# Kernel optimization log

Measured on AMD Instinct MI355X. Metric: run time of the kernel, lower is better.

The kernel has to match this reference:

```python
import jax, jax.numpy as jnp
import numpy as np

STRIDE = 16
SCALES = (0.5, 1.0, 2.0)
RATIOS = (0.5, 1.0, 2.0)
IOU_THR = 0.7
CONF_THR = 0.5
KEEP_PRE = 6000
KEEP_POST = 300


def _default_boxes(fh, fw):
    # anchors centered at origin: size = stride*scale, w/h set by aspect ratio
    s = STRIDE * jnp.asarray(SCALES, jnp.float32)                    # [S]
    r = jnp.asarray(RATIOS, jnp.float32)                             # [R]
    w = (s[None, :] * jnp.sqrt(1.0 / r)[:, None]).reshape(-1)        # [A]
    h = (s[None, :] * jnp.sqrt(r)[:, None]).reshape(-1)              # [A]
    anchors = jnp.stack([-w / 2, -h / 2, w / 2, h / 2], axis=-1)     # [A,4]
    sx = jnp.arange(fw, dtype=jnp.float32) * STRIDE
    sy = jnp.arange(fh, dtype=jnp.float32) * STRIDE
    gx, gy = jnp.meshgrid(sx, sy)                                    # [fh,fw]
    shifts = jnp.stack([gx, gy, gx, gy], axis=-1)                    # [fh,fw,4]
    return (shifts[:, :, None, :] + anchors[None, None, :, :]).reshape(-1, 4)


def _apply_regs(deltas, boxes):
    # deltas: [bs,N,4] (dx,dy,dw,dh); boxes: [N,4] xyxy default boxes
    w = boxes[:, 2] - boxes[:, 0]
    h = boxes[:, 3] - boxes[:, 1]
    cx = boxes[:, 0] + 0.5 * w
    cy = boxes[:, 1] + 0.5 * h
    pcx = deltas[..., 0] * w + cx
    pcy = deltas[..., 1] * h + cy
    pw = jnp.exp(deltas[..., 2]) * w
    ph = jnp.exp(deltas[..., 3]) * h
    return jnp.stack([pcx - 0.5 * pw, pcy - 0.5 * ph,
                      pcx + 0.5 * pw, pcy + 0.5 * ph], axis=-1)


def _clip(boxes, img_h, img_w):
    lim = jnp.asarray([img_w, img_h, img_w, img_h], jnp.float32)
    return jnp.clip(boxes, 0.0, lim)


def _pairwise_iou(b):
    area = jnp.maximum(b[:, 2] - b[:, 0], 0.0) * jnp.maximum(b[:, 3] - b[:, 1], 0.0)
    lt = jnp.maximum(b[:, None, :2], b[None, :, :2])
    rb = jnp.minimum(b[:, None, 2:], b[None, :, 2:])
    wh = jnp.maximum(rb - lt, 0.0)
    inter = wh[..., 0] * wh[..., 1]
    union = area[:, None] + area[None, :] - inter
    return inter / jnp.maximum(union, 1e-9)


def _nms_keep(boxes, thr):
    # boxes are pre-sorted by descending score -> greedy NMS == row sweep
    n = boxes.shape[0]
    iou = _pairwise_iou(jax.lax.stop_gradient(boxes))  # [n,n]
    idx = jnp.arange(n)
    def body(i, keep):
        sup = (iou[i] > thr) & (idx > i)
        return keep & jnp.where(keep[i], ~sup, True)
    return jax.lax.fori_loop(0, n, body, jnp.ones(n, dtype=bool))


def _detect_one(boxes, scores):
    order = jnp.argsort(-scores)
    props = boxes[order][:KEEP_PRE]          # [P,4]
    sc = scores[order][:KEEP_PRE]            # [P]
    keep = _nms_keep(props, IOU_THR)
    pos = jnp.cumsum(keep) - 1               # compacted position of kept boxes
    valid = keep & (pos < KEEP_POST)
    dst = jnp.where(valid, pos, KEEP_POST)   # out-of-range -> dropped by scatter
    out_b = jnp.zeros((KEEP_POST, 4), props.dtype).at[dst].set(props, mode='drop')
    out_s = jnp.zeros((KEEP_POST,), sc.dtype).at[dst].set(sc, mode='drop')
    # confidence filter: zero out rows below threshold (fixed-shape analog of list)
    return out_b * (out_s > CONF_THR).astype(props.dtype)[:, None]


def reference(preds, regs, img_h, img_w):
    bs, fh, fw, na = preds.shape
    db = _default_boxes(fh, fw)                          # [fh*fw*A, 4]
    scores = jax.nn.sigmoid(preds).reshape(bs, -1)       # [bs, N]
    boxes = _apply_regs(regs.reshape(bs, -1, 4), db)     # [bs, N, 4]
    boxes = _clip(boxes, img_h, img_w)
    outs = [_detect_one(boxes[i], scores[i]) for i in range(bs)]
    return jnp.stack(outs)                               # [bs, KEEP_POST, 4]


def setup_inputs() -> dict:
    key = jax.random.key(0)
    k1, k2 = jax.random.split(key)
    preds = jax.random.normal(k1, (4, 37, 62, 9), jnp.float32)
    regs = jax.random.normal(k2, (4, 37, 62, 9, 4), jnp.float32)
    return {"preds": preds, "regs": regs, "img_h": 600, "img_w": 1000}
```

## Files before the change

### kernel.cpp

```cpp
#include <hip/hip_runtime.h>
#include <stdint.h>

typedef unsigned long long u64;
typedef unsigned int u32;

#define FH 37
#define FW 62
#define NA 9
#define NPRED 20646
#define BS 4
#define KEEP_PRE 6000
#define KEEP_POST 300
#define NBINS 4096
#define SELCAP 3072
#define SLOTN 6144
#define FB_BASE 4608
#define NFB 640
#define NCHUNK 21
#define FSLOTS 32
#define FSUB 64

#define L_HIST   0u
#define L_SUF    16384u
#define L_RG1    32768u
#define L_RG2    81920u
#define L_FBCUR  106496u
#define L_PERM   109056u
#define L_KBOX   121344u
#define L_KAREA  126208u
#define L_WSUM   127424u
#define L_WPOS   127488u
#define L_SCAL   127552u
#define L_AW     127616u
#define L_MROW   127872u
#define LDS_TOTAL 128384u

__device__ __forceinline__ u32 mapbits(float p) {
  u32 u = __float_as_uint(p);
  return (u & 0x80000000u) ? ~u : (u | 0x80000000u);
}
__device__ __forceinline__ u64 readlane64(u64 v, int srcLane) {
  u32 lo = __builtin_amdgcn_readlane((u32)v, srcLane);
  u32 hi = __builtin_amdgcn_readlane((u32)(v >> 32), srcLane);
  return ((u64)hi << 32) | lo;
}
__device__ __forceinline__ bool iou_sup(float kx1, float ky1, float kx2, float ky2,
                                        float ka, float cx1, float cy1,
                                        float cx2, float cy2, float ca) {
  float wx = fmaxf(fminf(kx2, cx2) - fmaxf(kx1, cx1), 0.f);
  float wy = fmaxf(fminf(ky2, cy2) - fmaxf(ky1, cy1), 0.f);
  float inter = wx * wy;
  float un = ka + ca - inter;
  return inter > 0.7f * fmaxf(un, 1e-9f);
}
__device__ __forceinline__ float4 decode_box(u32 n, float4 d, float W, float H) {
  int a = (int)(n % NA);
  int cell = (int)(n / NA);
  int x = cell % FW;
  int y = cell / FW;
  int si = a % 3, ri = a / 3;
  float s = (si==0) ? 8.f : ((si==1) ? 16.f : 32.f);
  float r = (ri==0) ? 0.5f : ((ri==1) ? 1.0f : 2.0f);
  float aw = s * sqrtf(1.0f / r);
  float ah = s * sqrtf(r);
  float gx = (float)x * 16.f, gy = (float)y * 16.f;
  float x1d = gx - 0.5f*aw, x2d = gx + 0.5f*aw;
  float y1d = gy - 0.5f*ah, y2d = gy + 0.5f*ah;
  float w = x2d - x1d, h = y2d - y1d;
  float cx = x1d + 0.5f*w, cy = y1d + 0.5f*h;
  float pcx = d.x*w + cx, pcy = d.y*h + cy;
  float pw = expf(d.z)*w, ph = expf(d.w)*h;
  float bx1 = fminf(fmaxf(pcx - 0.5f*pw, 0.f), W);
  float by1 = fminf(fmaxf(pcy - 0.5f*ph, 0.f), H);
  float bx2 = fminf(fmaxf(pcx + 0.5f*pw, 0.f), W);
  float by2 = fminf(fmaxf(pcy + 0.5f*ph, 0.f), H);
  return make_float4(bx1, by1, bx2, by2);
}

__global__ void __launch_bounds__(1024) detect_kernel(
    const float* __restrict__ preds, const float4* __restrict__ regs4,
    const int* __restrict__ ih, const int* __restrict__ iw,
    float4* __restrict__ out)
{
  __shared__ __align__(16) char smem[LDS_TOTAL];
  u32*    histL  = (u32*)(smem + L_HIST);
  u32*    sufL   = (u32*)(smem + L_SUF);
  u32*    repl   = (u32*)(smem + L_RG1);
  u64*    slots  = (u64*)(smem + L_RG1);
  float4* cboxL  = (float4*)(smem + L_RG1);
  u32*    fineH  = (u32*)(smem + L_RG2);
  u32*    fineS  = (u32*)(smem + L_RG2 + 8192);
  u32*    fineC  = (u32*)(smem + L_RG2 + 16384);
  float*  careaL = (float*)(smem + L_RG2);
  u32*    fbCur  = (u32*)(smem + L_FBCUR);
  u32*    perm   = (u32*)(smem + L_PERM);
  float4* kbox   = (float4*)(smem + L_KBOX);
  float*  karea  = (float*)(smem + L_KAREA);
  u32*    wsum   = (u32*)(smem + L_WSUM);
  u32*    wpos   = (u32*)(smem + L_WPOS);
  u32*    scal   = (u32*)(smem + L_SCAL);
  u64*    aw     = (u64*)(smem + L_AW);
  u64*    mrow   = (u64*)(smem + L_MROW);

  const int b = blockIdx.x;
  const int t = threadIdx.x;
  const int lane = t & 63;
  const int wv = t >> 6;
  const float* pb = preds + b*NPRED;
  const float4* rb = regs4 + b*NPRED;
  const float W = (float)(*iw), H = (float)(*ih);
  float4* ob = out + b*KEEP_POST;
  const float4 zero = make_float4(0.f, 0.f, 0.f, 0.f);

  #pragma unroll
  for (int q = 0; q < 4; ++q) histL[q*1024 + t] = 0;
  #pragma unroll
  for (int q = 0; q < 12; ++q) repl[q*1024 + t] = 0;
  if (t == 0) scal[2] = 0;
  __syncthreads();

  {
    u32* repA = ((wv & 3) == 0) ? histL : (repl + ((wv & 3) - 1) * 4096);
    u32 mypos = 0;
    #pragma unroll 4
    for (int c = 0; c < NCHUNK; ++c) {
      int n = c*1024 + t;
      bool valid = (n < NPRED);
      float p = valid ? pb[n] : -1.0f;
      u64 bm = __ballot(valid && (p > 0.0f));
      mypos += (u32)__popcll(bm);
      if (valid) atomicAdd(&repA[mapbits(p) >> 20], 1u);
    }
    if (lane == 0) wpos[wv] = mypos;
  }
  __syncthreads();

  {
    u32* r2 = repl + 4096; u32* r3 = repl + 8192;
    u32 h0 = histL[4*t+0] + repl[4*t+0] + r2[4*t+0] + r3[4*t+0];
    u32 h1 = histL[4*t+1] + repl[4*t+1] + r2[4*t+1] + r3[4*t+1];
    u32 h2 = histL[4*t+2] + repl[4*t+2] + r2[4*t+2] + r3[4*t+2];
    u32 h3 = histL[4*t+3] + repl[4*t+3] + r2[4*t+3] + r3[4*t+3];
    histL[4*t+0]=h0; histL[4*t+1]=h1; histL[4*t+2]=h2; histL[4*t+3]=h3;
    u32 s = h0 + h1 + h2 + h3;
    u32 sf = s;
    #pragma unroll
    for (int off = 1; off < 64; off <<= 1) {
      u32 o = __shfl_down(sf, off, 64);
      if (lane + off < 64) sf += o;
    }
    if (lane == 0) wsum[wv] = sf;
    __syncthreads();
    u32 hi = 0;
    #pragma unroll
    for (int w2 = 0; w2 < 16; ++w2) hi += (w2 > wv) ? wsum[w2] : 0u;
    u32 St = hi + (sf - s);
    u32 s3 = St, s2 = s3 + h3, s1 = s2 + h2, s0 = s1 + h1;
    sufL[4*t+0]=s0; sufL[4*t+1]=s1; sufL[4*t+2]=s2; sufL[4*t+3]=s3;
    if (t == 0) {
      u32 np = 0;
      #pragma unroll
      for (int w2 = 0; w2 < 16; ++w2) np += wpos[w2];
      scal[3] = np;
    }
  }
  __syncthreads();

  #pragma unroll 1
  for (int tr = 0; tr < 2; ++tr) {
    const u32 winStart = (u32)tr * SELCAP;
    const u32 winEnd = winStart + SELCAP;
    const int rowLimit = (KEEP_PRE - (int)winStart < (int)SELCAP)
                           ? (KEEP_PRE - (int)winStart) : (int)SELCAP;

    if (t == 0) { scal[0] = 0xFFFFFFFFu; scal[1] = 0u; }
    __syncthreads();
    #pragma unroll
    for (int q = 0; q < 4; ++q) {
      int v = 4*t + q;
      u32 hv = histL[v], sv = sufL[v];
      if (hv && sv < winEnd && sv + hv > winStart) {
        atomicMin(&scal[0], (u32)v);
        atomicMax(&scal[1], (u32)v);
      }
    }
    __syncthreads();
    const u32 binLo = scal[0], binHi = scal[1];
    u32 cBase = binLo;
    if (binHi - binLo >= FSLOTS) cBase = binHi - (FSLOTS - 1);
    const u32 S_top = sufL[binHi];
    const u32 S_cb = (cBase > 0) ? sufL[cBase-1] : 0;
    const u32 rebWinEnd = winEnd - S_top;

    #pragma unroll
    for (int q = 0; q < 2; ++q) fineH[q*1024 + t] = 0;
    #pragma unroll
    for (int q = 0; q < 6; ++q) slots[q*1024 + t] = 0ull;
    if (t < NFB) {
      u32 v = binLo + (u32)t;
      fbCur[t] = (v < cBase) ? (FB_BASE + (sufL[v] - S_cb)) : (u32)SLOTN;
    }
    __syncthreads();

    #pragma unroll 4
    for (int c = 0; c < NCHUNK; ++c) {
      int n = c*1024 + t;
      if (n < NPRED) {
        u32 m = mapbits(pb[n]);
        u32 cb = m >> 20;
        if (cb >= cBase && cb <= binHi)
          atomicAdd(&fineH[((cb - cBase) << 6) | ((m >> 14) & 0x3F)], 1u);
      }
    }
    __syncthreads();

    {
      u32 f0 = fineH[2*t], f1 = fineH[2*t+1];
      u32 s = f0 + f1;
      u32 sf = s;
      #pragma unroll
      for (int off = 1; off < 64; off <<= 1) {
        u32 o = __shfl_down(sf, off, 64);
        if (lane + off < 64) sf += o;
      }
      if (lane == 0) wsum[wv] = sf;
      __syncthreads();
      u32 hi = 0;
      #pragma unroll
      for (int w2 = 0; w2 < 16; ++w2) hi += (w2 > wv) ? wsum[w2] : 0u;
      u32 St = hi + (sf - s);
      u32 sA = St + f1, sB = St;
      fineS[2*t] = sA; fineS[2*t+1] = sB;
      fineC[2*t] = sA; fineC[2*t+1] = sB;
    }
    __syncthreads();

    #pragma unroll 4
    for (int c = 0; c < NCHUNK; ++c) {
      int n = c*1024 + t;
      if (n < NPRED) {
        u32 m = mapbits(pb[n]);
        u32 cb = m >> 20;
        u64 key = ((u64)m << 32) | (u32)(~(u32)n);
        if (cb >= cBase && cb <= binHi) {
          u32 F = ((cb - cBase) << 6) | ((m >> 14) & 0x3F);
          if (fineS[F] < rebWinEnd) {
            u32 pos = atomicAdd(&fineC[F], 1u);
            if (pos < FB_BASE) slots[pos] = key;
          }
        } else if (cb >= binLo && cb < cBase) {
          u32 fo = cb - binLo;
          if (fo < NFB) {
            u32 pos = atomicAdd(&fbCur[fo], 1u);
            if (pos < SLOTN) slots[pos] = key;
          }
        }
      }
    }
    __syncthreads();

    #pragma unroll
    for (int q = 0; q < 6; ++q) {
      int i = q*1024 + t;
      u64 k = slots[i];
      if (k != 0) {
        u32 m = (u32)(k >> 32);
        u32 cb = m >> 20;
        u32 base, end, rbase;
        if (cb >= cBase) {
          u32 F = ((cb - cBase) << 6) | ((m >> 14) & 0x3F);
          base = fineS[F];
          end = base + fineH[F]; if (end > FB_BASE) end = FB_BASE;
          rbase = S_top + fineS[F];
        } else {
          base = FB_BASE + (sufL[cb] - S_cb);
          end = base + histL[cb]; if (end > SLOTN) end = SLOTN;
          rbase = sufL[cb];
        }
        u32 c2 = 0;
        for (u32 j = base; j < end; j += 4) {
          u64 s0 = slots[j];
          u64 s1 = (j+1 < end) ? slots[j+1] : 0ull;
          u64 s2 = (j+2 < end) ? slots[j+2] : 0ull;
          u64 s3 = (j+3 < end) ? slots[j+3] : 0ull;
          c2 += (u32)(s0 > k) + (u32)(s1 > k) + (u32)(s2 > k) + (u32)(s3 > k);
        }
        int local = (int)(rbase + c2) - (int)winStart;
        if (local >= 0 && local < rowLimit) perm[local] = ~(u32)k;
      }
    }
    __syncthreads();

    for (int r = t; r < rowLimit; r += 1024) {
      u32 idx = perm[r];
      float4 bx = decode_box(idx, rb[idx], W, H);
      cboxL[r] = bx;
      careaL[r] = (bx.z - bx.x) * (bx.w - bx.y);
    }
    __syncthreads();

    {
      const int npos = (int)scal[3];
      const int nblk = (rowLimit + 63) >> 6;
      for (int blk = 0; blk < nblk; ++blk) {
        int cnt = (int)scal[2];
        if (cnt >= KEEP_POST) break;
        const int base = blk * 64;
        const int ci = base + lane;
        const bool valid = (ci < rowLimit);
        float4 cur = cboxL[valid ? ci : 0];
        float carea = careaL[valid ? ci : 0];

        int dead = 0;
        #pragma unroll 2
        for (int k = wv; k < cnt; k += 16) {
          float4 kb = kbox[k];
          dead |= (int)iou_sup(kb.x, kb.y, kb.z, kb.w, karea[k],
                               cur.x, cur.y, cur.z, cur.w, carea);
        }
        u64* awb = aw + ((blk & 1) << 4);
        awb[wv] = __ballot(dead);
        __syncthreads();

        u64 deadAll = 0;
        #pragma unroll
        for (int k = 0; k < 16; ++k) deadAll |= awb[k];
        int rem = rowLimit - base;
        u64 vm = (rem >= 64) ? ~0ull : ((1ull << rem) - 1ull);
        u64 A = vm & ~deadAll;
        if (A == 0) continue;

        #pragma unroll
        for (int q = 0; q < 4; ++q) {
          int j = wv*4 + q;
          if ((A >> j) & 1ull) {
            float4 bj = cboxL[base + j];
            float ja = careaL[base + j];
            bool s = iou_sup(bj.x, bj.y, bj.z, bj.w, ja,
                             cur.x, cur.y, cur.z, cur.w, carea);
            u64 bm = __ballot(s);
            if (lane == 0) mrow[j] = bm;
          } else if (lane == 0) {
            mrow[j] = 0ull;
          }
        }
        __syncthreads();

        if (wv == 0) {
          u64 mreg = mrow[lane];
          int c2 = cnt;
          while (A && c2 < KEEP_POST) {
            int j = (int)__builtin_ctzll(A);
            A &= A - 1;
            A &= ~readlane64(mreg, j);
            if (lane == 0) {
              float4 bj = cboxL[base + j];
              kbox[c2] = bj;
              karea[c2] = careaL[base + j];
              ob[c2] = ((int)(winStart + (u32)(base + j)) < npos) ? bj : zero;
            }
            ++c2;
          }
          if (lane == 0) scal[2] = (u32)c2;
        }
        __syncthreads();
      }
    }
    __syncthreads();
    if ((int)scal[2] >= KEEP_POST) break;
  }

  for (int k2 = (int)scal[2] + t; k2 < KEEP_POST; k2 += 1024) ob[k2] = zero;
}

extern "C" void kernel_launch(void* const* d_in, const int* in_sizes, int n_in,
                              void* d_out, int out_size, void* d_ws, size_t ws_size,
                              hipStream_t stream) {
  const float* preds  = (const float*)d_in[0];
  const float4* regs4 = (const float4*)d_in[1];
  const int* ih       = (const int*)d_in[2];
  const int* iw       = (const int*)d_in[3];
  (void)d_ws; (void)ws_size; (void)in_sizes; (void)n_in; (void)out_size;

  detect_kernel<<<dim3(BS), 1024, 0, stream>>>(
      preds, regs4, ih, iw, (float4*)d_out);
}
```

Baseline: 174.2 us.

## Compact window candidates, split sort keys, lazily decode boxes, merge NMS barriers

The histogram pass now uses a single LDS histogram with no wave replicas, and the positive count is reduced with shuffles. The fine-histogram pass compacts in-window candidates into an LDS list through ballot and atomic offsets, so the scatter pass no longer rereads all predictions from global memory. Sort keys are split into 32-bit score bits plus 16-bit indices to save LDS. Box decoding is done for the first 1024 rows up front and the rest only when NMS reaches them. The intra-block suppression matrix is computed alongside the dead-mask pass so one barrier per block is removed, at the cost of always computing all 64 rows.

```diff
diff --git a/kernel.cpp b/kernel.cpp
--- a/kernel.cpp
+++ b/kernel.cpp
@@ -3,6 +3,7 @@
 
 typedef unsigned long long u64;
 typedef unsigned int u32;
+typedef unsigned short u16;
 
 #define FH 37
 #define FW 62
@@ -20,20 +21,27 @@
 #define FSLOTS 32
 #define FSUB 64
 
-#define L_HIST   0u
-#define L_SUF    16384u
-#define L_RG1    32768u
-#define L_RG2    81920u
-#define L_FBCUR  106496u
-#define L_PERM   109056u
-#define L_KBOX   121344u
-#define L_KAREA  126208u
-#define L_WSUM   127424u
-#define L_WPOS   127488u
-#define L_SCAL   127552u
-#define L_AW     127616u
-#define L_MROW   127872u
-#define LDS_TOTAL 128384u
+#define L_HIST    0u
+#define L_SUF     16384u
+#define L_C       32768u
+#define L_CM      (L_C + 0u)
+#define L_CN      (L_C + 24576u)
+#define L_FINEH   (L_C + 36864u)
+#define L_FINES   (L_C + 45056u)
+#define L_FINEC   (L_C + 53248u)
+#define L_FBCUR   (L_C + 61440u)
+#define L_CBOX    (L_C + 0u)
+#define L_CAREA   (L_C + 49152u)
+#define L_SLOTM   96768u
+#define L_SLOTN   121344u
+#define L_PERM    133632u
+#define L_KBOX    145920u
+#define L_KAREA   150720u
+#define L_WSUM    151920u
+#define L_SCAL    151984u
+#define L_AW      152016u
+#define L_MROW    152272u
+#define LDS_TOTAL 152832u
 
 __device__ __forceinline__ u32 mapbits(float p) {
   u32 u = __float_as_uint(p);
@@ -85,19 +93,20 @@
   __shared__ __align__(16) char smem[LDS_TOTAL];
   u32*    histL  = (u32*)(smem + L_HIST);
   u32*    sufL   = (u32*)(smem + L_SUF);
-  u32*    repl   = (u32*)(smem + L_RG1);
-  u64*    slots  = (u64*)(smem + L_RG1);
-  float4* cboxL  = (float4*)(smem + L_RG1);
-  u32*    fineH  = (u32*)(smem + L_RG2);
-  u32*    fineS  = (u32*)(smem + L_RG2 + 8192);
-  u32*    fineC  = (u32*)(smem + L_RG2 + 16384);
-  float*  careaL = (float*)(smem + L_RG2);
+  u32*    compM  = (u32*)(smem + L_CM);
+  u16*    compN  = (u16*)(smem + L_CN);
+  u32*    fineH  = (u32*)(smem + L_FINEH);
+  u32*    fineS  = (u32*)(smem + L_FINES);
+  u32*    fineC  = (u32*)(smem + L_FINEC);
   u32*    fbCur  = (u32*)(smem + L_FBCUR);
+  float4* cboxL  = (float4*)(smem + L_CBOX);
+  float*  careaL = (float*)(smem + L_CAREA);
+  u32*    slotM  = (u32*)(smem + L_SLOTM);
+  u16*    slotN  = (u16*)(smem + L_SLOTN);
   u32*    perm   = (u32*)(smem + L_PERM);
   float4* kbox   = (float4*)(smem + L_KBOX);
   float*  karea  = (float*)(smem + L_KAREA);
   u32*    wsum   = (u32*)(smem + L_WSUM);
-  u32*    wpos   = (u32*)(smem + L_WPOS);
   u32*    scal   = (u32*)(smem + L_SCAL);
   u64*    aw     = (u64*)(smem + L_AW);
   u64*    mrow   = (u64*)(smem + L_MROW);
@@ -112,57 +121,42 @@
   float4* ob = out + b*KEEP_POST;
   const float4 zero = make_float4(0.f, 0.f, 0.f, 0.f);
 
-  #pragma unroll
-  for (int q = 0; q < 4; ++q) histL[q*1024 + t] = 0;
-  #pragma unroll
-  for (int q = 0; q < 12; ++q) repl[q*1024 + t] = 0;
-  if (t == 0) scal[2] = 0;
+  ((uint4*)histL)[t] = make_uint4(0,0,0,0);
+  if (t == 0) { scal[2] = 0; scal[3] = 0; }
   __syncthreads();
 
-  {
-    u32* repA = ((wv & 3) == 0) ? histL : (repl + ((wv & 3) - 1) * 4096);
-    u32 mypos = 0;
-    #pragma unroll 4
-    for (int c = 0; c < NCHUNK; ++c) {
-      int n = c*1024 + t;
-      bool valid = (n < NPRED);
-      float p = valid ? pb[n] : -1.0f;
-      u64 bm = __ballot(valid && (p > 0.0f));
-      mypos += (u32)__popcll(bm);
-      if (valid) atomicAdd(&repA[mapbits(p) >> 20], 1u);
-    }
-    if (lane == 0) wpos[wv] = mypos;
+  u32 mypos = 0;
+  #pragma unroll 4
+  for (int c = 0; c < NCHUNK; ++c) {
+    int n = c*1024 + t;
+    if (n < NPRED) {
+      float p = pb[n];
+      mypos += (p > 0.0f) ? 1u : 0u;
+      atomicAdd(&histL[mapbits(p) >> 20], 1u);
+    }
   }
   __syncthreads();
 
   {
-    u32* r2 = repl + 4096; u32* r3 = repl + 8192;
-    u32 h0 = histL[4*t+0] + repl[4*t+0] + r2[4*t+0] + r3[4*t+0];
-    u32 h1 = histL[4*t+1] + repl[4*t+1] + r2[4*t+1] + r3[4*t+1];
-    u32 h2 = histL[4*t+2] + repl[4*t+2] + r2[4*t+2] + r3[4*t+2];
-    u32 h3 = histL[4*t+3] + repl[4*t+3] + r2[4*t+3] + r3[4*t+3];
-    histL[4*t+0]=h0; histL[4*t+1]=h1; histL[4*t+2]=h2; histL[4*t+3]=h3;
-    u32 s = h0 + h1 + h2 + h3;
+    uint4 h = ((const uint4*)histL)[t];
+    u32 s = h.x + h.y + h.z + h.w;
     u32 sf = s;
+    u32 mp = mypos;
     #pragma unroll
     for (int off = 1; off < 64; off <<= 1) {
       u32 o = __shfl_down(sf, off, 64);
       if (lane + off < 64) sf += o;
-    }
-    if (lane == 0) wsum[wv] = sf;
+      mp += __shfl_down(mp, off, 64);
+    }
+    if (lane == 0) { wsum[wv] = sf; atomicAdd(&scal[3], mp); }
     __syncthreads();
     u32 hi = 0;
     #pragma unroll
     for (int w2 = 0; w2 < 16; ++w2) hi += (w2 > wv) ? wsum[w2] : 0u;
     u32 St = hi + (sf - s);
-    u32 s3 = St, s2 = s3 + h3, s1 = s2 + h2, s0 = s1 + h1;
-    sufL[4*t+0]=s0; sufL[4*t+1]=s1; sufL[4*t+2]=s2; sufL[4*t+3]=s3;
-    if (t == 0) {
-      u32 np = 0;
-      #pragma unroll
-      for (int w2 = 0; w2 < 16; ++w2) np += wpos[w2];
-      scal[3] = np;
-    }
+    uint4 sv;
+    sv.w = St; sv.z = St + h.w; sv.y = sv.z + h.z; sv.x = sv.y + h.y;
+    ((uint4*)sufL)[t] = sv;
   }
   __syncthreads();
 
@@ -173,7 +167,7 @@
     const int rowLimit = (KEEP_PRE - (int)winStart < (int)SELCAP)
                            ? (KEEP_PRE - (int)winStart) : (int)SELCAP;
 
-    if (t == 0) { scal[0] = 0xFFFFFFFFu; scal[1] = 0u; }
+    if (t == 0) { scal[0] = 0xFFFFFFFFu; scal[1] = 0u; scal[4] = 0u; }
     __syncthreads();
     #pragma unroll
     for (int q = 0; q < 4; ++q) {
@@ -191,25 +185,42 @@
     const u32 S_top = sufL[binHi];
     const u32 S_cb = (cBase > 0) ? sufL[cBase-1] : 0;
     const u32 rebWinEnd = winEnd - S_top;
-
-    #pragma unroll
-    for (int q = 0; q < 2; ++q) fineH[q*1024 + t] = 0;
-    #pragma unroll
-    for (int q = 0; q < 6; ++q) slots[q*1024 + t] = 0ull;
+    const u32 fineCap = (cBase == binLo) ? (u32)SLOTN : (u32)FB_BASE;
+
+    fineH[2*t] = 0; fineH[2*t+1] = 0;
+    #pragma unroll
+    for (int q = 0; q < 6; ++q) slotM[q*1024 + t] = 0;
+    #pragma unroll
+    for (int q = 0; q < 3; ++q) ((u32*)slotN)[q*1024 + t] = 0;
     if (t < NFB) {
       u32 v = binLo + (u32)t;
       fbCur[t] = (v < cBase) ? (FB_BASE + (sufL[v] - S_cb)) : (u32)SLOTN;
     }
     __syncthreads();
 
-    #pragma unroll 4
+    #pragma unroll 2
     for (int c = 0; c < NCHUNK; ++c) {
       int n = c*1024 + t;
+      bool isWin = false;
+      u32 m = 0;
       if (n < NPRED) {
-        u32 m = mapbits(pb[n]);
+        m = mapbits(pb[n]);
         u32 cb = m >> 20;
+        isWin = (cb >= binLo && cb <= binHi);
         if (cb >= cBase && cb <= binHi)
           atomicAdd(&fineH[((cb - cBase) << 6) | ((m >> 14) & 0x3F)], 1u);
+      }
+      u64 bm = __ballot((int)isWin);
+      u32 cntw = (u32)__popcll(bm);
+      u32 basew = 0;
+      if (lane == 0) basew = atomicAdd(&scal[4], cntw);
+      basew = __builtin_amdgcn_readlane(basew, 0);
+      if (isWin) {
+        u32 pos = basew + (u32)__popcll(bm & ((1ull << lane) - 1ull));
+        if (pos < (u32)SLOTN) {
+          compM[pos] = m;
+          compN[pos] = (u16)(~(u32)n);
+        }
       }
     }
     __syncthreads();
@@ -235,24 +246,23 @@
     }
     __syncthreads();
 
-    #pragma unroll 4
-    for (int c = 0; c < NCHUNK; ++c) {
-      int n = c*1024 + t;
-      if (n < NPRED) {
-        u32 m = mapbits(pb[n]);
+    {
+      u32 tot = scal[4]; if (tot > (u32)SLOTN) tot = (u32)SLOTN;
+      for (u32 i = t; i < tot; i += 1024) {
+        u32 m = compM[i];
+        u16 nl = compN[i];
         u32 cb = m >> 20;
-        u64 key = ((u64)m << 32) | (u32)(~(u32)n);
-        if (cb >= cBase && cb <= binHi) {
+        if (cb >= cBase) {
           u32 F = ((cb - cBase) << 6) | ((m >> 14) & 0x3F);
           if (fineS[F] < rebWinEnd) {
             u32 pos = atomicAdd(&fineC[F], 1u);
-            if (pos < FB_BASE) slots[pos] = key;
+            if (pos < fineCap) { slotM[pos] = m; slotN[pos] = nl; }
           }
-        } else if (cb >= binLo && cb < cBase) {
+        } else {
           u32 fo = cb - binLo;
           if (fo < NFB) {
             u32 pos = atomicAdd(&fbCur[fo], 1u);
-            if (pos < SLOTN) slots[pos] = key;
+            if (pos < (u32)SLOTN) { slotM[pos] = m; slotN[pos] = nl; }
           }
         }
       }
@@ -262,40 +272,45 @@
     #pragma unroll
     for (int q = 0; q < 6; ++q) {
       int i = q*1024 + t;
-      u64 k = slots[i];
-      if (k != 0) {
-        u32 m = (u32)(k >> 32);
+      u32 m = slotM[i];
+      u16 nl = slotN[i];
+      if ((m | nl) != 0) {
         u32 cb = m >> 20;
         u32 base, end, rbase;
         if (cb >= cBase) {
           u32 F = ((cb - cBase) << 6) | ((m >> 14) & 0x3F);
           base = fineS[F];
-          end = base + fineH[F]; if (end > FB_BASE) end = FB_BASE;
+          end = base + fineH[F]; if (end > fineCap) end = fineCap;
           rbase = S_top + fineS[F];
         } else {
           base = FB_BASE + (sufL[cb] - S_cb);
-          end = base + histL[cb]; if (end > SLOTN) end = SLOTN;
+          end = base + histL[cb]; if (end > (u32)SLOTN) end = (u32)SLOTN;
           rbase = sufL[cb];
         }
         u32 c2 = 0;
         for (u32 j = base; j < end; j += 4) {
-          u64 s0 = slots[j];
-          u64 s1 = (j+1 < end) ? slots[j+1] : 0ull;
-          u64 s2 = (j+2 < end) ? slots[j+2] : 0ull;
-          u64 s3 = (j+3 < end) ? slots[j+3] : 0ull;
-          c2 += (u32)(s0 > k) + (u32)(s1 > k) + (u32)(s2 > k) + (u32)(s3 > k);
+          u32 m0 = slotM[j];                      u16 n0 = slotN[j];
+          u32 m1 = (j+1<end)?slotM[j+1]:0;        u16 n1 = (j+1<end)?slotN[j+1]:(u16)0;
+          u32 m2 = (j+2<end)?slotM[j+2]:0;        u16 n2 = (j+2<end)?slotN[j+2]:(u16)0;
+          u32 m3 = (j+3<end)?slotM[j+3]:0;        u16 n3 = (j+3<end)?slotN[j+3]:(u16)0;
+          c2 += (u32)((m0 > m) || (m0 == m && n0 > nl));
+          c2 += (u32)((m1 > m) || (m1 == m && n1 > nl));
+          c2 += (u32)((m2 > m) || (m2 == m && n2 > nl));
+          c2 += (u32)((m3 > m) || (m3 == m && n3 > nl));
         }
         int local = (int)(rbase + c2) - (int)winStart;
-        if (local >= 0 && local < rowLimit) perm[local] = ~(u32)k;
-      }
-    }
-    __syncthreads();
-
-    for (int r = t; r < rowLimit; r += 1024) {
-      u32 idx = perm[r];
+        if (local >= 0 && local < rowLimit)
+          perm[local] = (u32)((u16)(~nl));
+      }
+    }
+    __syncthreads();
+
+    int rowCap = (rowLimit < 1024) ? rowLimit : 1024;
+    if (t < rowCap) {
+      u32 idx = perm[t];
       float4 bx = decode_box(idx, rb[idx], W, H);
-      cboxL[r] = bx;
-      careaL[r] = (bx.z - bx.x) * (bx.w - bx.y);
+      cboxL[t] = bx;
+      careaL[t] = (bx.z - bx.x) * (bx.w - bx.y);
     }
     __syncthreads();
 
@@ -306,6 +321,20 @@
         int cnt = (int)scal[2];
         if (cnt >= KEEP_POST) break;
         const int base = blk * 64;
+
+        if (base + 64 > rowCap && base < rowLimit) {
+          int lo = rowCap;
+          int hi2 = rowCap + 2048; if (hi2 > rowLimit) hi2 = rowLimit;
+          for (int r = lo + t; r < hi2; r += 1024) {
+            u32 idx = perm[r];
+            float4 bx = decode_box(idx, rb[idx], W, H);
+            cboxL[r] = bx;
+            careaL[r] = (bx.z - bx.x) * (bx.w - bx.y);
+          }
+          rowCap = hi2;
+          __syncthreads();
+        }
+
         const int ci = base + lane;
         const bool valid = (ci < rowLimit);
         float4 cur = cboxL[valid ? ci : 0];
@@ -320,6 +349,18 @@
         }
         u64* awb = aw + ((blk & 1) << 4);
         awb[wv] = __ballot(dead);
+
+        #pragma unroll
+        for (int q = 0; q < 4; ++q) {
+          int j = wv*4 + q;
+          int jr = base + j; if (jr >= rowLimit) jr = 0;
+          float4 bj = cboxL[jr];
+          float ja = careaL[jr];
+          bool s = iou_sup(bj.x, bj.y, bj.z, bj.w, ja,
+                           cur.x, cur.y, cur.z, cur.w, carea);
+          u64 bm = __ballot(s);
+          if (lane == 0) mrow[j] = bm;
+        }
         __syncthreads();
 
         u64 deadAll = 0;
@@ -329,22 +370,6 @@
         u64 vm = (rem >= 64) ? ~0ull : ((1ull << rem) - 1ull);
         u64 A = vm & ~deadAll;
         if (A == 0) continue;
-
-        #pragma unroll
-        for (int q = 0; q < 4; ++q) {
-          int j = wv*4 + q;
-          if ((A >> j) & 1ull) {
-            float4 bj = cboxL[base + j];
-            float ja = careaL[base + j];
-            bool s = iou_sup(bj.x, bj.y, bj.z, bj.w, ja,
-                             cur.x, cur.y, cur.z, cur.w, carea);
-            u64 bm = __ballot(s);
-            if (lane == 0) mrow[j] = bm;
-          } else if (lane == 0) {
-            mrow[j] = 0ull;
-          }
-        }
-        __syncthreads();
 
         if (wv == 0) {
           u64 mreg = mrow[lane];
@@ -370,6 +395,7 @@
     if ((int)scal[2] >= KEEP_POST) break;
   }
 
+  __syncthreads();
   for (int k2 = (int)scal[2] + t; k2 < KEEP_POST; k2 += 1024) ob[k2] = zero;
 }
 
```

New measurement: 191.4 us. 1.1x slower.
